# Performance work log

Measured on AMD Instinct MI355X. Metric: run time of the kernel, lower is better.

The kernel has to match this reference:

```python
import jax, jax.numpy as jnp
import numpy as np

N_NODES = 100000


def gcn_conv(x, W, b, src, dst, deg_inv_sqrt):
    # PyG GCNConv: h = x @ W; msg = norm * h[src]; out = scatter_add at dst; out += b
    h = x @ W  # [N, H]
    norm = deg_inv_sqrt[src] * deg_inv_sqrt[dst]  # [E+N]
    msg = h[src] * norm[:, None]  # [E+N, H]
    out = jax.ops.segment_sum(msg, dst, num_segments=N_NODES)
    return out + b


def setup_inputs() -> dict:
    key = jax.random.key(0)
    k1, k2, k3, k4, k5, k6 = jax.random.split(key, 6)
    E = 1600000
    D_IN, H, D_OUT, L = 128, 128, 1, 3
    x = jax.random.normal(k1, (N_NODES, D_IN), dtype=jnp.float32)
    edge_index = jax.random.randint(k2, (2, E), 0, N_NODES, dtype=jnp.int64)
    # layer weights (input_size == hidden here, so stackable)
    scale = 1.0 / np.sqrt(H)
    Ws = jax.random.normal(k3, (L, D_IN, H), dtype=jnp.float32) * scale
    bs = jax.random.normal(k4, (L, H), dtype=jnp.float32) * 0.01
    Wf = jax.random.normal(k5, (H, D_OUT), dtype=jnp.float32) * scale
    bf = jax.random.normal(k6, (D_OUT,), dtype=jnp.float32) * 0.01
    return {"x": x, "edge_index": edge_index, "Ws": Ws, "bs": bs, "Wf": Wf, "bf": bf}


def reference(x, edge_index, Ws, bs, Wf, bf):
    # add self loops once (same graph for every layer)
    loop = jnp.arange(N_NODES, dtype=edge_index.dtype)
    src = jnp.concatenate([edge_index[0], loop])
    dst = jnp.concatenate([edge_index[1], loop])
    # symmetric normalization: deg counts incoming edges (incl. self loop)
    deg = jax.ops.segment_sum(jnp.ones_like(src, dtype=x.dtype), dst, num_segments=N_NODES)
    deg_inv_sqrt = jax.lax.rsqrt(deg)  # deg >= 1 thanks to self loops
    h = x
    for i in range(Ws.shape[0]):
        h = gcn_conv(h, Ws[i], bs[i], src, dst, deg_inv_sqrt)
        # dropout is identity in eval mode
        h = jax.nn.relu(h)
    return h @ Wf + bf
```

## Files before the change

### kernel.cpp

```cpp
#include <hip/hip_runtime.h>

#define DF 128
#define EB 4096

typedef short bf16x8 __attribute__((ext_vector_type(8)));
typedef float f32x4 __attribute__((ext_vector_type(4)));
typedef _Float16 h16x8 __attribute__((ext_vector_type(8)));

__device__ __forceinline__ float4 f4_relu(float4 v) {
    v.x = fmaxf(v.x, 0.f); v.y = fmaxf(v.y, 0.f); v.z = fmaxf(v.z, 0.f); v.w = fmaxf(v.w, 0.f);
    return v;
}
__device__ __forceinline__ unsigned short f32_to_bf16_rne(float f) {
    unsigned u = __float_as_uint(f);
    unsigned r = (u + 0x7fffu + ((u >> 16) & 1u)) >> 16;
    return (unsigned short)r;
}
__device__ __forceinline__ float bf16_to_f32(unsigned short h) {
    return __uint_as_float(((unsigned)h) << 16);
}
__device__ __forceinline__ void split8(float4 a, float4 b, bf16x8& hi, bf16x8& lo) {
    float v[8] = {a.x, a.y, a.z, a.w, b.x, b.y, b.z, b.w};
    #pragma unroll
    for (int j = 0; j < 8; ++j) {
        unsigned short h = f32_to_bf16_rne(v[j]);
        hi[j] = (short)h;
        float rem = v[j] - bf16_to_f32(h);
        lo[j] = (short)f32_to_bf16_rne(rem);
    }
}

__global__ __launch_bounds__(256) void p1a_hist(const int* __restrict__ ei, int E,
                                                int NBUKP, int* __restrict__ parthist) {
    __shared__ int hist[512];
    int t = threadIdx.x;
    for (int i = t; i < NBUKP; i += 256) hist[i] = 0;
    __syncthreads();
    int e0 = blockIdx.x * EB;
    #pragma unroll
    for (int j = 0; j < EB / 256; ++j) {
        int e = e0 + j * 256 + t;
        if (e < E) atomicAdd(&hist[ei[E + e] >> 8], 1);
    }
    __syncthreads();
    for (int i = t; i < NBUKP; i += 256)
        parthist[(size_t)blockIdx.x * NBUKP + i] = hist[i];
}

__global__ __launch_bounds__(256) void colscan_kernel(int* __restrict__ parthist,
                                                      int NBLK, int NBUKP,
                                                      int* __restrict__ btotal) {
    __shared__ int wsum[4];
    int k = blockIdx.x;
    int t = threadIdx.x;
    int Q = (NBLK + 255) / 256;
    int b0 = t * Q;
    int local[8];
    int s = 0;
    for (int j = 0; j < Q; ++j) {
        int b = b0 + j;
        int v = (b < NBLK) ? parthist[(size_t)b * NBUKP + k] : 0;
        local[j] = v;
        s += v;
    }
    int lane = t & 63, wid = t >> 6;
    int incl = s;
    #pragma unroll
    for (int off = 1; off < 64; off <<= 1) {
        int n = __shfl_up(incl, off, 64);
        if (lane >= off) incl += n;
    }
    if (lane == 63) wsum[wid] = incl;
    __syncthreads();
    int wbase = 0, total = 0;
    #pragma unroll
    for (int w = 0; w < 4; ++w) {
        int v = wsum[w];
        if (w < wid) wbase += v;
        total += v;
    }
    int run = wbase + incl - s;
    for (int j = 0; j < Q; ++j) {
        int b = b0 + j;
        if (b < NBLK) parthist[(size_t)b * NBUKP + k] = run;
        run += local[j];
    }
    if (t == 0) btotal[k] = total;
}

__global__ __launch_bounds__(1024) void scan_offsets_kernel(int* __restrict__ partials, int NB,
                                                            int* __restrict__ scan_end) {
    __shared__ int wtot[16];
    int t = threadIdx.x, lane = t & 63, wid = t >> 6;
    int c = (t < NB) ? partials[t] : 0;
    int incl = c;
    #pragma unroll
    for (int off = 1; off < 64; off <<= 1) {
        int n = __shfl_up(incl, off, 64);
        if (lane >= off) incl += n;
    }
    if (lane == 63) wtot[wid] = incl;
    __syncthreads();
    int wbase = 0, total = 0;
    #pragma unroll
    for (int w = 0; w < 16; ++w) {
        int v = wtot[w];
        if (w < wid) wbase += v;
        total += v;
    }
    if (t < NB) partials[t] = wbase + incl - c;
    if (t == 0) *scan_end = total;
}

__global__ __launch_bounds__(256) void p1c_scatter(const int* __restrict__ ei, int E,
                                                   int NBUK, int NBUKP,
                                                   const int* __restrict__ parthist,
                                                   const int* __restrict__ bbase,
                                                   unsigned int* __restrict__ pbuf) {
    __shared__ int cur[512];
    int t = threadIdx.x;
    for (int i = t; i < NBUK; i += 256)
        cur[i] = bbase[i] + parthist[(size_t)blockIdx.x * NBUKP + i];
    __syncthreads();
    int e0 = blockIdx.x * EB;
    #pragma unroll
    for (int j = 0; j < EB / 256; ++j) {
        int e = e0 + j * 256 + t;
        if (e < E) {
            int s = ei[e], d = ei[E + e];
            int pos = atomicAdd(&cur[d >> 8], 1);
            pbuf[pos] = ((unsigned)s << 8) | (unsigned)(d & 255);
        }
    }
}

__global__ __launch_bounds__(256) void p2_csr(const unsigned int* __restrict__ pbuf,
                                              const int* __restrict__ bbase,
                                              int N, int E,
                                              int* __restrict__ edges4,
                                              int* __restrict__ row_start,
                                              float* __restrict__ dis) {
    __shared__ int hist[256];
    __shared__ int cur[256];
    __shared__ int wsum[4];
    int k = blockIdx.x, t = threadIdx.x;
    int gbase = bbase[k], gend = bbase[k + 1];
    hist[t] = 0;
    __syncthreads();
    for (int p = gbase + t; p < gend; p += 256)
        atomicAdd(&hist[pbuf[p] & 255], 1);
    __syncthreads();
    int c = hist[t];
    int lane = t & 63, wid = t >> 6;
    int incl = c;
    #pragma unroll
    for (int off = 1; off < 64; off <<= 1) {
        int n = __shfl_up(incl, off, 64);
        if (lane >= off) incl += n;
    }
    if (lane == 63) wsum[wid] = incl;
    __syncthreads();
    int wbase = 0;
    #pragma unroll
    for (int w = 0; w < 4; ++w)
        if (w < wid) wbase += wsum[w];
    int excl = wbase + incl - c;
    int id = k * 256 + t;
    if (id < N) {
        row_start[id] = gbase + excl;
        dis[id] = rsqrtf((float)(c + 1));
    }
    if (k == 0 && t == 0) row_start[N] = E;
    cur[t] = gbase + excl;
    __syncthreads();
    for (int p = gbase + t; p < gend; p += 256) {
        unsigned rec = pbuf[p];
        int pos = atomicAdd(&cur[rec & 255], 1);
        edges4[pos] = (int)(rec >> 8);
    }
}

__global__ __launch_bounds__(256) void wprep_kernel(const float* __restrict__ Ws,
                                                    unsigned short* __restrict__ WHg,
                                                    unsigned short* __restrict__ WLg,
                                                    int total) {
    int g = blockIdx.x * 256 + threadIdx.x;
    if (g >= total) return;
    int l = g >> 11;
    int t = g & 2047;
    int s = t >> 9;
    int n = (t >> 6) & 7;
    int lane = t & 63;
    int kb = s * 32 + ((lane >> 4) << 2);
    int c  = n * 16 + (lane & 15);
    const float* W = Ws + (size_t)l * DF * DF;
    bf16x8 hi, lo;
    #pragma unroll
    for (int j = 0; j < 8; ++j) {
        int k = kb + (j & 3) + ((j >> 2) << 4);
        float w = W[k * DF + c];
        unsigned short h = f32_to_bf16_rne(w);
        hi[j] = (short)h;
        lo[j] = (short)f32_to_bf16_rne(w - bf16_to_f32(h));
    }
    *(bf16x8*)&WHg[(size_t)g * 8] = hi;
    *(bf16x8*)&WLg[(size_t)g * 8] = lo;
}

#define GBM 128
__global__ __launch_bounds__(256) void gemm_mfma(const float* __restrict__ A,
                                                 const unsigned short* __restrict__ WHg,
                                                 const unsigned short* __restrict__ WLg,
                                                 const float* __restrict__ dis,
                                                 _Float16* __restrict__ C,
                                                 int M, int relu) {
    int tid  = threadIdx.x;
    int wid  = tid >> 6;
    int lane = tid & 63;
    int l15  = lane & 15;
    int l4   = lane >> 4;
    size_t row0 = (size_t)blockIdx.x * GBM + wid * 32;

    f32x4 acc[2][8];
    #pragma unroll
    for (int tr = 0; tr < 2; ++tr)
        #pragma unroll
        for (int n = 0; n < 8; ++n) acc[tr][n] = (f32x4)(0.f);

    const float* Ar0 = A + (row0 + l15) * DF;
    const float* Ar1 = A + (row0 + 16 + l15) * DF;
    bool ok0 = (row0 + l15) < (size_t)M;
    bool ok1 = (row0 + 16 + l15) < (size_t)M;
    float4 zero = make_float4(0.f, 0.f, 0.f, 0.f);

    #pragma unroll
    for (int s = 0; s < 4; ++s) {
        int c0 = s * 32 + l4 * 4;
        float4 a00 = ok0 ? *(const float4*)&Ar0[c0]      : zero;
        float4 a01 = ok0 ? *(const float4*)&Ar0[c0 + 16] : zero;
        float4 a10 = ok1 ? *(const float4*)&Ar1[c0]      : zero;
        float4 a11 = ok1 ? *(const float4*)&Ar1[c0 + 16] : zero;
        if (relu) {
            a00 = f4_relu(a00); a01 = f4_relu(a01);
            a10 = f4_relu(a10); a11 = f4_relu(a11);
        }
        bf16x8 ah0, al0, ah1, al1;
        split8(a00, a01, ah0, al0);
        split8(a10, a11, ah1, al1);
        #pragma unroll
        for (int n = 0; n < 8; ++n) {
            size_t g = (size_t)((s * 8 + n) * 64 + lane) * 8;
            bf16x8 bh = *(const bf16x8*)&WHg[g];
            bf16x8 bl = *(const bf16x8*)&WLg[g];
            acc[0][n] = __builtin_amdgcn_mfma_f32_16x16x32_bf16(ah0, bh, acc[0][n], 0, 0, 0);
            acc[0][n] = __builtin_amdgcn_mfma_f32_16x16x32_bf16(ah0, bl, acc[0][n], 0, 0, 0);
            acc[0][n] = __builtin_amdgcn_mfma_f32_16x16x32_bf16(al0, bh, acc[0][n], 0, 0, 0);
            acc[1][n] = __builtin_amdgcn_mfma_f32_16x16x32_bf16(ah1, bh, acc[1][n], 0, 0, 0);
            acc[1][n] = __builtin_amdgcn_mfma_f32_16x16x32_bf16(ah1, bl, acc[1][n], 0, 0, 0);
            acc[1][n] = __builtin_amdgcn_mfma_f32_16x16x32_bf16(al1, bh, acc[1][n], 0, 0, 0);
        }
    }

    #pragma unroll
    for (int tr = 0; tr < 2; ++tr) {
        size_t rbase = row0 + tr * 16 + l4 * 4;
        #pragma unroll
        for (int q = 0; q < 4; ++q) {
            size_t r = rbase + q;
            if (r < (size_t)M) {
                float ds = dis[r];
                #pragma unroll
                for (int n = 0; n < 8; ++n)
                    C[r * DF + n * 16 + l15] = (_Float16)(acc[tr][n][q] * ds);
            }
        }
    }
}

template <int FINAL>
__global__ __launch_bounds__(256) void agg_kernel(const _Float16* __restrict__ g,
                                                  const int* __restrict__ edges4,
                                                  const int* __restrict__ row_start,
                                                  const float* __restrict__ dis,
                                                  const float* __restrict__ bias,
                                                  const float* __restrict__ Wf,
                                                  const float* __restrict__ bf,
                                                  float* __restrict__ out, int N) {
    int gid = blockIdx.x * 16 + (threadIdx.x >> 4);
    int l8  = threadIdx.x & 15;
    if (gid >= N) return;
    const h16x8* gv = (const h16x8*)g;
    float acc[8];
    {
        h16x8 self = gv[(size_t)gid * 16 + l8];
        #pragma unroll
        for (int j = 0; j < 8; ++j) acc[j] = (float)self[j];
    }
    int s = row_start[gid], e = row_start[gid + 1];
    int p = s;
    for (; p + 4 <= e; p += 4) {
        int s0 = edges4[p];
        int s1 = edges4[p + 1];
        int s2 = edges4[p + 2];
        int s3 = edges4[p + 3];
        h16x8 v0 = gv[(size_t)s0 * 16 + l8];
        h16x8 v1 = gv[(size_t)s1 * 16 + l8];
        h16x8 v2 = gv[(size_t)s2 * 16 + l8];
        h16x8 v3 = gv[(size_t)s3 * 16 + l8];
        #pragma unroll
        for (int j = 0; j < 8; ++j)
            acc[j] += (float)v0[j] + (float)v1[j] + (float)v2[j] + (float)v3[j];
    }
    for (; p < e; ++p) {
        h16x8 v = gv[(size_t)edges4[p] * 16 + l8];
        #pragma unroll
        for (int j = 0; j < 8; ++j) acc[j] += (float)v[j];
    }
    float d = dis[gid];
    if (FINAL) {
        float pr = 0.f;
        #pragma unroll
        for (int j = 0; j < 8; ++j) {
            float v = fmaxf(acc[j] * d + bias[l8 * 8 + j], 0.f);
            pr += v * Wf[l8 * 8 + j];
        }
        #pragma unroll
        for (int off = 8; off > 0; off >>= 1) pr += __shfl_xor(pr, off, 16);
        if (l8 == 0) out[gid] = pr + bf[0];
    } else {
        float4 o0, o1;
        o0.x = acc[0] * d + bias[l8 * 8 + 0];
        o0.y = acc[1] * d + bias[l8 * 8 + 1];
        o0.z = acc[2] * d + bias[l8 * 8 + 2];
        o0.w = acc[3] * d + bias[l8 * 8 + 3];
        o1.x = acc[4] * d + bias[l8 * 8 + 4];
        o1.y = acc[5] * d + bias[l8 * 8 + 5];
        o1.z = acc[6] * d + bias[l8 * 8 + 6];
        o1.w = acc[7] * d + bias[l8 * 8 + 7];
        float4* op = (float4*)&out[(size_t)gid * DF + l8 * 8];
        op[0] = o0;
        op[1] = o1;
    }
}

extern "C" void kernel_launch(void* const* d_in, const int* in_sizes, int n_in,
                              void* d_out, int out_size, void* d_ws, size_t ws_size,
                              hipStream_t stream) {
    const float* x  = (const float*)d_in[0];
    const int*   ei = (const int*)d_in[1];
    const float* Ws = (const float*)d_in[2];
    const float* bs = (const float*)d_in[3];
    const float* Wf = (const float*)d_in[4];
    const float* bf = (const float*)d_in[5];
    float* out = (float*)d_out;

    int N = in_sizes[0] / DF;
    int E = in_sizes[1] / 2;
    int L = in_sizes[2] / (DF * DF);

    int NBUK  = (N + 255) >> 8;
    int NBUKP = NBUK + 1;
    int NBLK  = (E + EB - 1) / EB;

    char* p = (char*)d_ws;
    auto alloc = [&](size_t bytes) {
        char* r = p;
        p += (bytes + 255) & ~(size_t)255;
        return r;
    };
    int*   row_start = (int*)alloc((size_t)(N + 1) * 4);
    float* dis       = (float*)alloc((size_t)N * 4);
    int*   edges4    = (int*)alloc((size_t)E * 4);
    unsigned int* pbuf = (unsigned int*)alloc((size_t)E * 4);
    int*   parthist  = (int*)alloc((size_t)NBLK * NBUKP * 4);
    int*   btotal    = (int*)alloc((size_t)(NBUK + 1) * 4);
    _Float16* bufG   = (_Float16*)alloc((size_t)N * DF * 2);
    float* bufB      = (float*)alloc((size_t)N * DF * 4);
    unsigned short* WHg = (unsigned short*)alloc((size_t)L * 2048 * 8 * 2);
    unsigned short* WLg = (unsigned short*)alloc((size_t)L * 2048 * 8 * 2);

    int WT = L * 2048;

    wprep_kernel<<<(WT + 255) / 256, 256, 0, stream>>>(Ws, WHg, WLg, WT);
    p1a_hist<<<NBLK, 256, 0, stream>>>(ei, E, NBUKP, parthist);
    colscan_kernel<<<NBUK, 256, 0, stream>>>(parthist, NBLK, NBUKP, btotal);
    scan_offsets_kernel<<<1, 1024, 0, stream>>>(btotal, NBUK, &btotal[NBUK]);
    p1c_scatter<<<NBLK, 256, 0, stream>>>(ei, E, NBUK, NBUKP, parthist, btotal, pbuf);
    p2_csr<<<NBUK, 256, 0, stream>>>(pbuf, btotal, N, E, edges4, row_start, dis);

    const float* hin = x;
    for (int l = 0; l < L; ++l) {
        gemm_mfma<<<(N + GBM - 1) / GBM, 256, 0, stream>>>(
            hin, WHg + (size_t)l * 16384, WLg + (size_t)l * 16384, dis, bufG, N, l > 0);
        if (l == L - 1) {
            agg_kernel<1><<<(N + 15) / 16, 256, 0, stream>>>(bufG, edges4, row_start, dis,
                                                             bs + (size_t)l * DF, Wf, bf, out, N);
        } else {
            agg_kernel<0><<<(N + 15) / 16, 256, 0, stream>>>(bufG, edges4, row_start, dis,
                                                             bs + (size_t)l * DF, nullptr, nullptr,
                                                             bufB, N);
            hin = bufB;
        }
    }
}
```

Measured before the change: 472.4 us.

## Store GEMM output in feature-sliced planes and aggregate per slice

The GEMM now writes its fp16 output as 8 planes of 16 features each instead of row-major 128-wide rows. Aggregation runs one block per slice per group of 64 nodes, so each gather touches a 1.6 MB plane that fits in cache better than the full 25 MB matrix. The fused final projection moves into a separate final_kernel that reads the fp32 layer output back. In exchange, edge indices and row offsets are read 8 times, each gather fetches only 8 bytes, and the last layer adds an extra fp32 write and read.

```diff
diff --git a/kernel.cpp b/kernel.cpp
--- a/kernel.cpp
+++ b/kernel.cpp
@@ -5,7 +5,7 @@
 
 typedef short bf16x8 __attribute__((ext_vector_type(8)));
 typedef float f32x4 __attribute__((ext_vector_type(4)));
-typedef _Float16 h16x8 __attribute__((ext_vector_type(8)));
+typedef _Float16 h16x4 __attribute__((ext_vector_type(4)));
 
 __device__ __forceinline__ float4 f4_relu(float4 v) {
     v.x = fmaxf(v.x, 0.f); v.y = fmaxf(v.y, 0.f); v.z = fmaxf(v.z, 0.f); v.w = fmaxf(v.w, 0.f);
@@ -212,7 +212,7 @@
                                                  const unsigned short* __restrict__ WHg,
                                                  const unsigned short* __restrict__ WLg,
                                                  const float* __restrict__ dis,
-                                                 _Float16* __restrict__ C,
+                                                 _Float16* __restrict__ gs,
                                                  int M, int relu) {
     int tid  = threadIdx.x;
     int wid  = tid >> 6;
@@ -261,6 +261,7 @@
         }
     }
 
+    size_t plane = (size_t)M * 16;
     #pragma unroll
     for (int tr = 0; tr < 2; ++tr) {
         size_t rbase = row0 + tr * 16 + l4 * 4;
@@ -271,76 +272,77 @@
                 float ds = dis[r];
                 #pragma unroll
                 for (int n = 0; n < 8; ++n)
-                    C[r * DF + n * 16 + l15] = (_Float16)(acc[tr][n][q] * ds);
+                    gs[(size_t)n * plane + r * 16 + l15] = (_Float16)(acc[tr][n][q] * ds);
             }
         }
     }
 }
 
-template <int FINAL>
-__global__ __launch_bounds__(256) void agg_kernel(const _Float16* __restrict__ g,
-                                                  const int* __restrict__ edges4,
-                                                  const int* __restrict__ row_start,
-                                                  const float* __restrict__ dis,
-                                                  const float* __restrict__ bias,
-                                                  const float* __restrict__ Wf,
-                                                  const float* __restrict__ bf,
-                                                  float* __restrict__ out, int N) {
-    int gid = blockIdx.x * 16 + (threadIdx.x >> 4);
-    int l8  = threadIdx.x & 15;
+__global__ __launch_bounds__(256) void agg_slice(const _Float16* __restrict__ gs,
+                                                 const int* __restrict__ edges4,
+                                                 const int* __restrict__ row_start,
+                                                 const float* __restrict__ dis,
+                                                 const float* __restrict__ bias,
+                                                 float* __restrict__ outB, int N) {
+    int bid = blockIdx.x;
+    int s   = bid & 7;
+    int gid = (bid >> 3) * 64 + (threadIdx.x >> 2);
+    int fl  = threadIdx.x & 3;
     if (gid >= N) return;
-    const h16x8* gv = (const h16x8*)g;
-    float acc[8];
+    const h16x4* gv = (const h16x4*)gs + (size_t)s * N * 4;
+    float acc[4];
     {
-        h16x8 self = gv[(size_t)gid * 16 + l8];
-        #pragma unroll
-        for (int j = 0; j < 8; ++j) acc[j] = (float)self[j];
-    }
-    int s = row_start[gid], e = row_start[gid + 1];
-    int p = s;
-    for (; p + 4 <= e; p += 4) {
+        h16x4 self = gv[(size_t)gid * 4 + fl];
+        #pragma unroll
+        for (int j = 0; j < 4; ++j) acc[j] = (float)self[j];
+    }
+    int e0 = row_start[gid], e1 = row_start[gid + 1];
+    int p = e0;
+    for (; p + 4 <= e1; p += 4) {
         int s0 = edges4[p];
         int s1 = edges4[p + 1];
         int s2 = edges4[p + 2];
         int s3 = edges4[p + 3];
-        h16x8 v0 = gv[(size_t)s0 * 16 + l8];
-        h16x8 v1 = gv[(size_t)s1 * 16 + l8];
-        h16x8 v2 = gv[(size_t)s2 * 16 + l8];
-        h16x8 v3 = gv[(size_t)s3 * 16 + l8];
-        #pragma unroll
-        for (int j = 0; j < 8; ++j)
+        h16x4 v0 = gv[(size_t)s0 * 4 + fl];
+        h16x4 v1 = gv[(size_t)s1 * 4 + fl];
+        h16x4 v2 = gv[(size_t)s2 * 4 + fl];
+        h16x4 v3 = gv[(size_t)s3 * 4 + fl];
+        #pragma unroll
+        for (int j = 0; j < 4; ++j)
             acc[j] += (float)v0[j] + (float)v1[j] + (float)v2[j] + (float)v3[j];
     }
-    for (; p < e; ++p) {
-        h16x8 v = gv[(size_t)edges4[p] * 16 + l8];
-        #pragma unroll
-        for (int j = 0; j < 8; ++j) acc[j] += (float)v[j];
+    for (; p < e1; ++p) {
+        h16x4 v = gv[(size_t)edges4[p] * 4 + fl];
+        #pragma unroll
+        for (int j = 0; j < 4; ++j) acc[j] += (float)v[j];
     }
     float d = dis[gid];
-    if (FINAL) {
-        float pr = 0.f;
-        #pragma unroll
-        for (int j = 0; j < 8; ++j) {
-            float v = fmaxf(acc[j] * d + bias[l8 * 8 + j], 0.f);
-            pr += v * Wf[l8 * 8 + j];
-        }
-        #pragma unroll
-        for (int off = 8; off > 0; off >>= 1) pr += __shfl_xor(pr, off, 16);
-        if (l8 == 0) out[gid] = pr + bf[0];
-    } else {
-        float4 o0, o1;
-        o0.x = acc[0] * d + bias[l8 * 8 + 0];
-        o0.y = acc[1] * d + bias[l8 * 8 + 1];
-        o0.z = acc[2] * d + bias[l8 * 8 + 2];
-        o0.w = acc[3] * d + bias[l8 * 8 + 3];
-        o1.x = acc[4] * d + bias[l8 * 8 + 4];
-        o1.y = acc[5] * d + bias[l8 * 8 + 5];
-        o1.z = acc[6] * d + bias[l8 * 8 + 6];
-        o1.w = acc[7] * d + bias[l8 * 8 + 7];
-        float4* op = (float4*)&out[(size_t)gid * DF + l8 * 8];
-        op[0] = o0;
-        op[1] = o1;
-    }
+    int f0 = s * 16 + fl * 4;
+    float4 o;
+    o.x = acc[0] * d + bias[f0 + 0];
+    o.y = acc[1] * d + bias[f0 + 1];
+    o.z = acc[2] * d + bias[f0 + 2];
+    o.w = acc[3] * d + bias[f0 + 3];
+    *(float4*)&outB[(size_t)gid * DF + f0] = o;
+}
+
+__global__ __launch_bounds__(256) void final_kernel(const float* __restrict__ h,
+                                                    const float* __restrict__ Wf,
+                                                    const float* __restrict__ bf,
+                                                    float* __restrict__ out, int N) {
+    int gid = blockIdx.x * 16 + (threadIdx.x >> 4);
+    int l8  = threadIdx.x & 15;
+    if (gid >= N) return;
+    const float4* hp = (const float4*)&h[(size_t)gid * DF + l8 * 8];
+    float4 a = f4_relu(hp[0]);
+    float4 b = f4_relu(hp[1]);
+    const float4* wp = (const float4*)&Wf[l8 * 8];
+    float4 wa = wp[0], wb = wp[1];
+    float pr = a.x * wa.x + a.y * wa.y + a.z * wa.z + a.w * wa.w
+             + b.x * wb.x + b.y * wb.y + b.z * wb.z + b.w * wb.w;
+    #pragma unroll
+    for (int off = 8; off > 0; off >>= 1) pr += __shfl_xor(pr, off, 16);
+    if (l8 == 0) out[gid] = pr + bf[0];
 }
 
 extern "C" void kernel_launch(void* const* d_in, const int* in_sizes, int n_in,
@@ -388,18 +390,14 @@
     p1c_scatter<<<NBLK, 256, 0, stream>>>(ei, E, NBUK, NBUKP, parthist, btotal, pbuf);
     p2_csr<<<NBUK, 256, 0, stream>>>(pbuf, btotal, N, E, edges4, row_start, dis);
 
+    int agg_grid = ((N + 63) / 64) * 8;
     const float* hin = x;
     for (int l = 0; l < L; ++l) {
         gemm_mfma<<<(N + GBM - 1) / GBM, 256, 0, stream>>>(
             hin, WHg + (size_t)l * 16384, WLg + (size_t)l * 16384, dis, bufG, N, l > 0);
-        if (l == L - 1) {
-            agg_kernel<1><<<(N + 15) / 16, 256, 0, stream>>>(bufG, edges4, row_start, dis,
-                                                             bs + (size_t)l * DF, Wf, bf, out, N);
-        } else {
-            agg_kernel<0><<<(N + 15) / 16, 256, 0, stream>>>(bufG, edges4, row_start, dis,
-                                                             bs + (size_t)l * DF, nullptr, nullptr,
-                                                             bufB, N);
-            hin = bufB;
-        }
-    }
-}
+        agg_slice<<<agg_grid, 256, 0, stream>>>(bufG, edges4, row_start, dis,
+                                                bs + (size_t)l * DF, bufB, N);
+        hin = bufB;
+    }
+    final_kernel<<<(N + 15) / 16, 256, 0, stream>>>(bufB, Wf, bf, out, N);
+}
```

Result: slower. 561.2 us (+18.8%).

## Store inter-layer activations in fp16 and fuse ReLU into aggregation

Applied to the files above, without the earlier changes.

Layer activations are now stored in fp16 rather than fp32. A new conversion kernel turns the input x into fp16, and the aggregation kernel applies bias and ReLU before writing fp16 output, so the GEMM reads half as many bytes and no longer does its own ReLU. The weight-prep K layout is changed to match contiguous 8-element fp16 loads, and edge index loads become nontemporal. This cuts memory traffic between GEMM and aggregation, but adds an extra pass over x and lowers the precision of the activations fed to the GEMM.

```diff
diff --git a/kernel.cpp b/kernel.cpp
--- a/kernel.cpp
+++ b/kernel.cpp
@@ -7,10 +7,6 @@
 typedef float f32x4 __attribute__((ext_vector_type(4)));
 typedef _Float16 h16x8 __attribute__((ext_vector_type(8)));
 
-__device__ __forceinline__ float4 f4_relu(float4 v) {
-    v.x = fmaxf(v.x, 0.f); v.y = fmaxf(v.y, 0.f); v.z = fmaxf(v.z, 0.f); v.w = fmaxf(v.w, 0.f);
-    return v;
-}
 __device__ __forceinline__ unsigned short f32_to_bf16_rne(float f) {
     unsigned u = __float_as_uint(f);
     unsigned r = (u + 0x7fffu + ((u >> 16) & 1u)) >> 16;
@@ -19,14 +15,13 @@
 __device__ __forceinline__ float bf16_to_f32(unsigned short h) {
     return __uint_as_float(((unsigned)h) << 16);
 }
-__device__ __forceinline__ void split8(float4 a, float4 b, bf16x8& hi, bf16x8& lo) {
-    float v[8] = {a.x, a.y, a.z, a.w, b.x, b.y, b.z, b.w};
+__device__ __forceinline__ void split8h(h16x8 a, bf16x8& hi, bf16x8& lo) {
     #pragma unroll
     for (int j = 0; j < 8; ++j) {
-        unsigned short h = f32_to_bf16_rne(v[j]);
+        float v = (float)a[j];
+        unsigned short h = f32_to_bf16_rne(v);
         hi[j] = (short)h;
-        float rem = v[j] - bf16_to_f32(h);
-        lo[j] = (short)f32_to_bf16_rne(rem);
+        lo[j] = (short)f32_to_bf16_rne(v - bf16_to_f32(h));
     }
 }
 
@@ -180,6 +175,18 @@
     }
 }
 
+__global__ __launch_bounds__(256) void x16_kernel(const float* __restrict__ x,
+                                                  _Float16* __restrict__ x16, size_t total8) {
+    size_t i = (size_t)blockIdx.x * 256 + threadIdx.x;
+    if (i >= total8) return;
+    const float4* xp = (const float4*)&x[i * 8];
+    float4 a = xp[0], b = xp[1];
+    h16x8 o;
+    o[0] = (_Float16)a.x; o[1] = (_Float16)a.y; o[2] = (_Float16)a.z; o[3] = (_Float16)a.w;
+    o[4] = (_Float16)b.x; o[5] = (_Float16)b.y; o[6] = (_Float16)b.z; o[7] = (_Float16)b.w;
+    *(h16x8*)&x16[i * 8] = o;
+}
+
 __global__ __launch_bounds__(256) void wprep_kernel(const float* __restrict__ Ws,
                                                     unsigned short* __restrict__ WHg,
                                                     unsigned short* __restrict__ WLg,
@@ -191,13 +198,13 @@
     int s = t >> 9;
     int n = (t >> 6) & 7;
     int lane = t & 63;
-    int kb = s * 32 + ((lane >> 4) << 2);
+    int kb = s * 32 + ((lane >> 4) << 3);
     int c  = n * 16 + (lane & 15);
     const float* W = Ws + (size_t)l * DF * DF;
     bf16x8 hi, lo;
     #pragma unroll
     for (int j = 0; j < 8; ++j) {
-        int k = kb + (j & 3) + ((j >> 2) << 4);
+        int k = kb + j;
         float w = W[k * DF + c];
         unsigned short h = f32_to_bf16_rne(w);
         hi[j] = (short)h;
@@ -208,12 +215,12 @@
 }
 
 #define GBM 128
-__global__ __launch_bounds__(256) void gemm_mfma(const float* __restrict__ A,
+__global__ __launch_bounds__(256) void gemm_mfma(const _Float16* __restrict__ A,
                                                  const unsigned short* __restrict__ WHg,
                                                  const unsigned short* __restrict__ WLg,
                                                  const float* __restrict__ dis,
                                                  _Float16* __restrict__ C,
-                                                 int M, int relu) {
+                                                 int M) {
     int tid  = threadIdx.x;
     int wid  = tid >> 6;
     int lane = tid & 63;
@@ -227,26 +234,19 @@
         #pragma unroll
         for (int n = 0; n < 8; ++n) acc[tr][n] = (f32x4)(0.f);
 
-    const float* Ar0 = A + (row0 + l15) * DF;
-    const float* Ar1 = A + (row0 + 16 + l15) * DF;
+    const _Float16* Ar0 = A + (row0 + l15) * DF;
+    const _Float16* Ar1 = A + (row0 + 16 + l15) * DF;
     bool ok0 = (row0 + l15) < (size_t)M;
     bool ok1 = (row0 + 16 + l15) < (size_t)M;
-    float4 zero = make_float4(0.f, 0.f, 0.f, 0.f);
 
     #pragma unroll
     for (int s = 0; s < 4; ++s) {
-        int c0 = s * 32 + l4 * 4;
-        float4 a00 = ok0 ? *(const float4*)&Ar0[c0]      : zero;
-        float4 a01 = ok0 ? *(const float4*)&Ar0[c0 + 16] : zero;
-        float4 a10 = ok1 ? *(const float4*)&Ar1[c0]      : zero;
-        float4 a11 = ok1 ? *(const float4*)&Ar1[c0 + 16] : zero;
-        if (relu) {
-            a00 = f4_relu(a00); a01 = f4_relu(a01);
-            a10 = f4_relu(a10); a11 = f4_relu(a11);
-        }
+        int c0 = s * 32 + l4 * 8;
+        h16x8 a0 = ok0 ? *(const h16x8*)&Ar0[c0] : (h16x8)(_Float16)0;
+        h16x8 a1 = ok1 ? *(const h16x8*)&Ar1[c0] : (h16x8)(_Float16)0;
         bf16x8 ah0, al0, ah1, al1;
-        split8(a00, a01, ah0, al0);
-        split8(a10, a11, ah1, al1);
+        split8h(a0, ah0, al0);
+        split8h(a1, ah1, al1);
         #pragma unroll
         for (int n = 0; n < 8; ++n) {
             size_t g = (size_t)((s * 8 + n) * 64 + lane) * 8;
@@ -285,7 +285,7 @@
                                                   const float* __restrict__ bias,
                                                   const float* __restrict__ Wf,
                                                   const float* __restrict__ bf,
-                                                  float* __restrict__ out, int N) {
+                                                  void* __restrict__ out, int N) {
     int gid = blockIdx.x * 16 + (threadIdx.x >> 4);
     int l8  = threadIdx.x & 15;
     if (gid >= N) return;
@@ -299,10 +299,10 @@
     int s = row_start[gid], e = row_start[gid + 1];
     int p = s;
     for (; p + 4 <= e; p += 4) {
-        int s0 = edges4[p];
-        int s1 = edges4[p + 1];
-        int s2 = edges4[p + 2];
-        int s3 = edges4[p + 3];
+        int s0 = __builtin_nontemporal_load(&edges4[p]);
+        int s1 = __builtin_nontemporal_load(&edges4[p + 1]);
+        int s2 = __builtin_nontemporal_load(&edges4[p + 2]);
+        int s3 = __builtin_nontemporal_load(&edges4[p + 3]);
         h16x8 v0 = gv[(size_t)s0 * 16 + l8];
         h16x8 v1 = gv[(size_t)s1 * 16 + l8];
         h16x8 v2 = gv[(size_t)s2 * 16 + l8];
@@ -312,7 +312,8 @@
             acc[j] += (float)v0[j] + (float)v1[j] + (float)v2[j] + (float)v3[j];
     }
     for (; p < e; ++p) {
-        h16x8 v = gv[(size_t)edges4[p] * 16 + l8];
+        int s0 = __builtin_nontemporal_load(&edges4[p]);
+        h16x8 v = gv[(size_t)s0 * 16 + l8];
         #pragma unroll
         for (int j = 0; j < 8; ++j) acc[j] += (float)v[j];
     }
@@ -326,20 +327,13 @@
         }
         #pragma unroll
         for (int off = 8; off > 0; off >>= 1) pr += __shfl_xor(pr, off, 16);
-        if (l8 == 0) out[gid] = pr + bf[0];
+        if (l8 == 0) ((float*)out)[gid] = pr + bf[0];
     } else {
-        float4 o0, o1;
-        o0.x = acc[0] * d + bias[l8 * 8 + 0];
-        o0.y = acc[1] * d + bias[l8 * 8 + 1];
-        o0.z = acc[2] * d + bias[l8 * 8 + 2];
-        o0.w = acc[3] * d + bias[l8 * 8 + 3];
-        o1.x = acc[4] * d + bias[l8 * 8 + 4];
-        o1.y = acc[5] * d + bias[l8 * 8 + 5];
-        o1.z = acc[6] * d + bias[l8 * 8 + 6];
-        o1.w = acc[7] * d + bias[l8 * 8 + 7];
-        float4* op = (float4*)&out[(size_t)gid * DF + l8 * 8];
-        op[0] = o0;
-        op[1] = o1;
+        h16x8 o;
+        #pragma unroll
+        for (int j = 0; j < 8; ++j)
+            o[j] = (_Float16)fmaxf(acc[j] * d + bias[l8 * 8 + j], 0.f);
+        *(h16x8*)&((_Float16*)out)[(size_t)gid * DF + l8 * 8] = o;
     }
 }
 
@@ -374,32 +368,32 @@
     unsigned int* pbuf = (unsigned int*)alloc((size_t)E * 4);
     int*   parthist  = (int*)alloc((size_t)NBLK * NBUKP * 4);
     int*   btotal    = (int*)alloc((size_t)(NBUK + 1) * 4);
+    _Float16* bufA16 = (_Float16*)alloc((size_t)N * DF * 2);
     _Float16* bufG   = (_Float16*)alloc((size_t)N * DF * 2);
-    float* bufB      = (float*)alloc((size_t)N * DF * 4);
     unsigned short* WHg = (unsigned short*)alloc((size_t)L * 2048 * 8 * 2);
     unsigned short* WLg = (unsigned short*)alloc((size_t)L * 2048 * 8 * 2);
 
     int WT = L * 2048;
+    size_t total8 = (size_t)N * DF / 8;
 
     wprep_kernel<<<(WT + 255) / 256, 256, 0, stream>>>(Ws, WHg, WLg, WT);
+    x16_kernel<<<(int)((total8 + 255) / 256), 256, 0, stream>>>(x, bufA16, total8);
     p1a_hist<<<NBLK, 256, 0, stream>>>(ei, E, NBUKP, parthist);
     colscan_kernel<<<NBUK, 256, 0, stream>>>(parthist, NBLK, NBUKP, btotal);
     scan_offsets_kernel<<<1, 1024, 0, stream>>>(btotal, NBUK, &btotal[NBUK]);
     p1c_scatter<<<NBLK, 256, 0, stream>>>(ei, E, NBUK, NBUKP, parthist, btotal, pbuf);
     p2_csr<<<NBUK, 256, 0, stream>>>(pbuf, btotal, N, E, edges4, row_start, dis);
 
-    const float* hin = x;
     for (int l = 0; l < L; ++l) {
         gemm_mfma<<<(N + GBM - 1) / GBM, 256, 0, stream>>>(
-            hin, WHg + (size_t)l * 16384, WLg + (size_t)l * 16384, dis, bufG, N, l > 0);
+            bufA16, WHg + (size_t)l * 16384, WLg + (size_t)l * 16384, dis, bufG, N);
         if (l == L - 1) {
             agg_kernel<1><<<(N + 15) / 16, 256, 0, stream>>>(bufG, edges4, row_start, dis,
                                                              bs + (size_t)l * DF, Wf, bf, out, N);
         } else {
             agg_kernel<0><<<(N + 15) / 16, 256, 0, stream>>>(bufG, edges4, row_start, dis,
                                                              bs + (size_t)l * DF, nullptr, nullptr,
-                                                             bufB, N);
-            hin = bufB;
-        }
-    }
-}
+                                                             bufA16, N);
+        }
+    }
+}
```

Result: faster. 438.9 us (-7.1%).
